# Kernel tuning notes

Measured on AMD Instinct MI355X. Metric: run time of the kernel, lower is better.

Reference implementation:

```python
import jax, jax.numpy as jnp
import numpy as np

V, D, NH, L, T, B = 32000, 768, 12, 4, 2048, 1
HD = D // NH
THETA = 10000.0
EPS = 1e-5


def setup_inputs() -> dict:
    key = jax.random.key(0)
    ks = jax.random.split(key, 12)
    s = 0.02
    return {
        "idx": jax.random.randint(ks[0], (B, T), 0, V),
        "wte": jax.random.normal(ks[1], (V, D), jnp.float32) * s,
        "ln1_w": jnp.ones((L, D), jnp.float32),
        "attn_w": jax.random.normal(ks[2], (L, 3 * D, D), jnp.float32) * s,
        "attnproj_w": jax.random.normal(ks[3], (L, D, D), jnp.float32) * s,
        "ln2_w": jnp.ones((L, D), jnp.float32),
        "fc_w": jax.random.normal(ks[4], (L, 4 * D, D), jnp.float32) * s,
        "fc_b": jnp.zeros((L, 4 * D), jnp.float32),
        "proj_w": jax.random.normal(ks[5], (L, D, 4 * D), jnp.float32) * s,
        "proj_b": jnp.zeros((L, D), jnp.float32),
        "lnf_w": jnp.ones((D,), jnp.float32),
        "unemb_b": jnp.zeros((V,), jnp.float32),
    }


def _ln(x, w):
    mu = jnp.mean(x, axis=-1, keepdims=True)
    var = jnp.mean(jnp.square(x - mu), axis=-1, keepdims=True)
    return (x - mu) * jax.lax.rsqrt(var + EPS) * w


def _rope(x, cos, sin):
    # x: [B,NH,T,HD]; cos/sin: [T,HD//2]
    x1, x2 = x[..., : HD // 2], x[..., HD // 2 :]
    return jnp.concatenate([x1 * cos - x2 * sin, x1 * sin + x2 * cos], axis=-1)


def _forward(idx, wte, ln1_w, attn_w, attnproj_w, ln2_w, fc_w, fc_b, proj_w, proj_b, lnf_w, unemb_b):
    x = wte[idx]  # [B,T,D]
    inv_freq = 1.0 / (THETA ** (jnp.arange(0, HD, 2, dtype=jnp.float32) / HD))  # [HD/2]
    t = jnp.arange(T, dtype=jnp.float32)
    freqs = jnp.outer(t, inv_freq)  # [T, HD/2]
    cos, sin = jnp.cos(freqs), jnp.sin(freqs)
    causal = jnp.tril(jnp.ones((T, T), bool))
    scale = 1.0 / jnp.sqrt(jnp.asarray(HD, x.dtype))
    for l in range(L):
        h = _ln(x, ln1_w[l])
        qkv = h @ attn_w[l].T  # [B,T,3D]
        q, k, v = jnp.split(qkv, 3, axis=-1)
        q = q.reshape(B, T, NH, HD).transpose(0, 2, 1, 3)
        k = k.reshape(B, T, NH, HD).transpose(0, 2, 1, 3)
        v = v.reshape(B, T, NH, HD).transpose(0, 2, 1, 3)
        q, k = _rope(q, cos, sin), _rope(k, cos, sin)
        att = jnp.einsum("bhqd,bhkd->bhqk", q, k) * scale
        att = jnp.where(causal, att, -jnp.inf)
        att = jax.nn.softmax(att, axis=-1)
        y = jnp.einsum("bhqk,bhkd->bhqd", att, v)
        y = y.transpose(0, 2, 1, 3).reshape(B, T, D)
        x = x + y @ attnproj_w[l].T
        h = _ln(x, ln2_w[l])
        m = jax.nn.gelu(h @ fc_w[l].T + fc_b[l], approximate=False)
        x = x + m @ proj_w[l].T + proj_b[l]
    x = _ln(x, lnf_w)
    return x @ wte.T + unemb_b  # tied unembedding, [B,T,V]


def reference(idx, wte, ln1_w, attn_w, attnproj_w, ln2_w, fc_w, fc_b, proj_w, proj_b, lnf_w, unemb_b):
    return _forward(idx, wte, ln1_w, attn_w, attnproj_w, ln2_w, fc_w, fc_b, proj_w, proj_b, lnf_w, unemb_b)
```

## Files before the change

### kernel.cpp

```cpp
#include <hip/hip_runtime.h>
#include <hip/hip_bf16.h>

typedef __bf16 bf16_t;
typedef __bf16 bf16x8 __attribute__((ext_vector_type(8)));
typedef __bf16 bf16x4 __attribute__((ext_vector_type(4)));
typedef float  f32x4  __attribute__((ext_vector_type(4)));

__device__ __forceinline__ void gl_lds16(const void* g, void* l) {
    __builtin_amdgcn_global_load_lds(
        (__attribute__((address_space(1))) void*)g,
        (__attribute__((address_space(3))) void*)l, 16, 0, 0);
}

__global__ void cvt_kernel(const float* __restrict__ in, bf16_t* __restrict__ out,
                           int n4) {
    const int i = blockIdx.x * 256 + threadIdx.x;
    if (i < n4) {
        const float4 v = ((const float4*)in)[i];
        bf16x4 o;
        o.x = (bf16_t)v.x; o.y = (bf16_t)v.y; o.z = (bf16_t)v.z; o.w = (bf16_t)v.w;
        ((bf16x4*)out)[i] = o;
    }
}

__global__ void embed_kernel(const int* __restrict__ idx,
                             const float* __restrict__ wte,
                             float* __restrict__ x) {
    const int t = blockIdx.x;
    const int row = idx[t];
    const float* w = wte + (size_t)row * 768;
    float* o = x + (size_t)t * 768;
    for (int d = threadIdx.x; d < 768; d += 256) o[d] = w[d];
}

__global__ __launch_bounds__(256) void ln_kernel(const float* __restrict__ x,
                                                 const float* __restrict__ w,
                                                 bf16_t* __restrict__ out) {
    const int t = blockIdx.x, tid = threadIdx.x;
    __shared__ float red[256];
    const float* xr = x + (size_t)t * 768;
    const float v0 = xr[tid], v1 = xr[tid + 256], v2 = xr[tid + 512];
    red[tid] = v0 + v1 + v2;
    __syncthreads();
    for (int s = 128; s > 0; s >>= 1) {
        if (tid < s) red[tid] += red[tid + s];
        __syncthreads();
    }
    const float mu = red[0] * (1.0f / 768.0f);
    __syncthreads();
    const float d0 = v0 - mu, d1 = v1 - mu, d2 = v2 - mu;
    red[tid] = d0 * d0 + d1 * d1 + d2 * d2;
    __syncthreads();
    for (int s = 128; s > 0; s >>= 1) {
        if (tid < s) red[tid] += red[tid + s];
        __syncthreads();
    }
    const float rstd = rsqrtf(red[0] * (1.0f / 768.0f) + 1e-5f);
    bf16_t* orow = out + (size_t)t * 768;
    orow[tid]       = (bf16_t)(d0 * rstd * w[tid]);
    orow[tid + 256] = (bf16_t)(d1 * rstd * w[tid + 256]);
    orow[tid + 512] = (bf16_t)(d2 * rstd * w[tid + 512]);
}

__global__ __launch_bounds__(256) void rope_prep(const float* __restrict__ qkv,
                                                 bf16_t* __restrict__ Qb,
                                                 bf16_t* __restrict__ Kb,
                                                 bf16_t* __restrict__ Vt) {
    const int t0 = blockIdx.x * 64, h = blockIdx.y;
    const int tid = threadIdx.x;
    __shared__ bf16_t vt[64][65];

    #pragma unroll
    for (int it = 0; it < 16; ++it) {
        const int item = it * 256 + tid;
        const int tl = item >> 6;
        const int which = (item >> 5) & 1;
        const int i = item & 31;
        const float* src = qkv + (size_t)(t0 + tl) * 2304 + which * 768 + h * 64;
        const float inv_freq = __powf(10000.0f, -(float)i * (1.0f / 32.0f));
        const float ang = (float)(t0 + tl) * inv_freq;
        float s, c;
        __sincosf(ang, &s, &c);
        const float x1 = src[i], x2 = src[i + 32];
        bf16_t* dst = (which ? Kb : Qb) + ((size_t)h * 2048 + t0 + tl) * 64;
        const float sc = which ? 1.0f : 0.125f;
        dst[i]      = (bf16_t)((x1 * c - x2 * s) * sc);
        dst[i + 32] = (bf16_t)((x1 * s + x2 * c) * sc);
    }

    #pragma unroll
    for (int pass = 0; pass < 4; ++pass) {
        const int r = pass * 16 + (tid >> 4);
        const int c = (tid & 15) * 4;
        const float4 v = *(const float4*)(qkv + (size_t)(t0 + r) * 2304 + 1536 + h * 64 + c);
        vt[c + 0][r] = (bf16_t)v.x;
        vt[c + 1][r] = (bf16_t)v.y;
        vt[c + 2][r] = (bf16_t)v.z;
        vt[c + 3][r] = (bf16_t)v.w;
    }
    __syncthreads();
    #pragma unroll
    for (int pass = 0; pass < 2; ++pass) {
        const int d = pass * 32 + (tid >> 3);
        const int k8 = (tid & 7) * 8;
        bf16x8 vv;
        #pragma unroll
        for (int j = 0; j < 8; ++j) vv[j] = vt[d][k8 + j];
        *(bf16x8*)(Vt + ((size_t)h * 64 + d) * 2048 + t0 + k8) = vv;
    }
}

__global__ __launch_bounds__(256) void attn_mfma(const bf16_t* __restrict__ Qb,
                                                 const bf16_t* __restrict__ Kb,
                                                 const bf16_t* __restrict__ Vt,
                                                 bf16_t* __restrict__ y) {
    const int qt = (int)gridDim.x - 1 - (int)blockIdx.x;
    const int h  = blockIdx.y;
    const int q0 = qt * 64;
    const int tid = threadIdx.x;
    const int w = tid >> 6, lane = tid & 63;
    const int lg = lane >> 4;
    const int ll = lane & 15;

    __shared__ bf16_t Ks[64 * 64];
    __shared__ bf16_t Vs[64 * 64];
    __shared__ bf16_t Ps[64 * 64];

    bf16x8 aq0, aq1;
    {
        const bf16_t* qp = Qb + ((size_t)h * 2048 + q0 + w * 16 + ll) * 64 + lg * 8;
        aq0 = *(const bf16x8*)qp;
        aq1 = *(const bf16x8*)(qp + 32);
    }

    f32x4 o[4];
    #pragma unroll
    for (int i = 0; i < 4; ++i) o[i] = (f32x4)(0.0f);
    float m_i[4], l_i[4];
    #pragma unroll
    for (int r = 0; r < 4; ++r) { m_i[r] = -3e38f; l_i[r] = 0.0f; }

    const int srow0 = tid >> 3;
    const int srow1 = srow0 + 32;
    const int sc16  = tid & 7;

    const bf16_t* Kbase = Kb + (size_t)h * 2048 * 64;
    const bf16_t* Vbase = Vt + (size_t)h * 64 * 2048;

    for (int kt = 0; kt <= qt; ++kt) {
        __syncthreads();
        {
            const bf16_t* kg = Kbase + (size_t)(kt * 64) * 64;
            const bf16x8 k0 = *(const bf16x8*)(kg + srow0 * 64 + sc16 * 8);
            const bf16x8 k1 = *(const bf16x8*)(kg + srow1 * 64 + sc16 * 8);
            const bf16_t* vg = Vbase + kt * 64;
            const bf16x8 v0 = *(const bf16x8*)(vg + (size_t)srow0 * 2048 + sc16 * 8);
            const bf16x8 v1 = *(const bf16x8*)(vg + (size_t)srow1 * 2048 + sc16 * 8);
            *(bf16x8*)((char*)(Ks + srow0 * 64) + ((sc16 * 16) ^ ((srow0 & 7) << 4))) = k0;
            *(bf16x8*)((char*)(Ks + srow1 * 64) + ((sc16 * 16) ^ ((srow1 & 7) << 4))) = k1;
            *(bf16x8*)((char*)(Vs + srow0 * 64) + ((sc16 * 16) ^ ((srow0 & 7) << 4))) = v0;
            *(bf16x8*)((char*)(Vs + srow1 * 64) + ((sc16 * 16) ^ ((srow1 & 7) << 4))) = v1;
        }
        __syncthreads();

        f32x4 sacc[4];
        #pragma unroll
        for (int kb = 0; kb < 4; ++kb) {
            const int krow = kb * 16 + ll;
            const char* kr = (const char*)(Ks + krow * 64);
            const int sw = (krow & 7) << 4;
            const bf16x8 b0 = *(const bf16x8*)(kr + ((lg * 16) ^ sw));
            const bf16x8 b1 = *(const bf16x8*)(kr + ((64 + lg * 16) ^ sw));
            sacc[kb] = __builtin_amdgcn_mfma_f32_16x16x32_bf16(aq0, b0, (f32x4)(0.0f), 0, 0, 0);
            sacc[kb] = __builtin_amdgcn_mfma_f32_16x16x32_bf16(aq1, b1, sacc[kb], 0, 0, 0);
        }

        float sc_[4][4];
        const bool diag = (kt == qt);
        #pragma unroll
        for (int kb = 0; kb < 4; ++kb) {
            #pragma unroll
            for (int r = 0; r < 4; ++r) {
                float v = sacc[kb][r];
                if (diag && (kb * 16 + ll) > (w * 16 + lg * 4 + r)) v = -3e38f;
                sc_[kb][r] = v;
            }
        }
        float rmax[4];
        #pragma unroll
        for (int r = 0; r < 4; ++r)
            rmax[r] = fmaxf(fmaxf(sc_[0][r], sc_[1][r]), fmaxf(sc_[2][r], sc_[3][r]));
        #pragma unroll
        for (int st = 0; st < 4; ++st) {
            const int off = 1 << st;
            #pragma unroll
            for (int r = 0; r < 4; ++r)
                rmax[r] = fmaxf(rmax[r], __shfl_xor(rmax[r], off));
        }
        float alpha[4], rsum[4];
        #pragma unroll
        for (int r = 0; r < 4; ++r) {
            const float mn = fmaxf(m_i[r], rmax[r]);
            alpha[r] = __expf(m_i[r] - mn);
            m_i[r] = mn;
            rsum[r] = 0.0f;
        }
        #pragma unroll
        for (int kb = 0; kb < 4; ++kb) {
            #pragma unroll
            for (int r = 0; r < 4; ++r) {
                const float p = __expf(sc_[kb][r] - m_i[r]);
                sc_[kb][r] = p;
                rsum[r] += p;
            }
        }
        #pragma unroll
        for (int st = 0; st < 4; ++st) {
            const int off = 1 << st;
            #pragma unroll
            for (int r = 0; r < 4; ++r)
                rsum[r] += __shfl_xor(rsum[r], off);
        }
        #pragma unroll
        for (int r = 0; r < 4; ++r) l_i[r] = l_i[r] * alpha[r] + rsum[r];

        #pragma unroll
        for (int r = 0; r < 4; ++r) {
            const int prow = w * 16 + lg * 4 + r;
            char* pb = (char*)(Ps + prow * 64);
            const int sw = (prow & 7) << 4;
            #pragma unroll
            for (int kb = 0; kb < 4; ++kb)
                *(bf16_t*)(pb + (((kb * 16 + ll) * 2) ^ sw)) = (bf16_t)sc_[kb][r];
        }

        #pragma unroll
        for (int db = 0; db < 4; ++db)
            #pragma unroll
            for (int r = 0; r < 4; ++r) o[db][r] *= alpha[r];

        #pragma unroll
        for (int ks = 0; ks < 2; ++ks) {
            const int arow = w * 16 + ll;
            const bf16x8 ap = *(const bf16x8*)((const char*)(Ps + arow * 64) +
                                ((ks * 64 + lg * 16) ^ ((arow & 7) << 4)));
            #pragma unroll
            for (int db = 0; db < 4; ++db) {
                const int vrow = db * 16 + ll;
                const bf16x8 bv = *(const bf16x8*)((const char*)(Vs + vrow * 64) +
                                    ((ks * 64 + lg * 16) ^ ((vrow & 7) << 4)));
                o[db] = __builtin_amdgcn_mfma_f32_16x16x32_bf16(ap, bv, o[db], 0, 0, 0);
            }
        }
    }

    #pragma unroll
    for (int r = 0; r < 4; ++r) {
        const float inv = 1.0f / l_i[r];
        bf16_t* yo = y + (size_t)(q0 + w * 16 + lg * 4 + r) * 768 + h * 64 + ll;
        #pragma unroll
        for (int db = 0; db < 4; ++db)
            yo[db * 16] = (bf16_t)(o[db][r] * inv);
    }
}

template <int FLAGS, int BM>
__global__ __launch_bounds__(256) void gemm_bt(const bf16_t* __restrict__ A,
                                               const bf16_t* __restrict__ B,
                                               const float* __restrict__ bias,
                                               float* __restrict__ C32,
                                               bf16_t* __restrict__ Cb,
                                               int M, int N, int K) {
    constexpr bool HAS_BIAS = (FLAGS & 1) != 0;
    constexpr bool HAS_RES  = (FLAGS & 2) != 0;
    constexpr bool HAS_GELU = (FLAGS & 4) != 0;
    constexpr bool OUT_BF16 = (FLAGS & 8) != 0;
    constexpr bool UNEMB    = (FLAGS & 16) != 0;
    constexpr int  WM       = (BM == 128) ? 64 : 32;
    constexpr int  MI       = WM / 16;

    __shared__ bf16_t As[BM * 32];
    __shared__ bf16_t Bs[128 * 32];

    const int tid = threadIdx.x;
    const int w = tid >> 6, lane = tid & 63;
    const int bm = (UNEMB ? blockIdx.x : blockIdx.y) * BM;
    const int bn = (UNEMB ? blockIdx.y : blockIdx.x) * 128;
    const int wm = (w >> 1) * WM, wn = (w & 1) * 64;

    const int sc = (lane & 3) * 8;
    const int srB = w * 32 + (lane >> 2);
    const bf16_t* gB0 = B + (size_t)(bn + srB) * K + sc;
    const bf16_t* gB1 = gB0 + (size_t)16 * K;
    bf16_t* lB0 = Bs + (w * 32) * 32;
    bf16_t* lB1 = lB0 + 16 * 32;
    const int srA = (BM == 128) ? srB : (w * 16 + (lane >> 2));
    const bf16_t* gA0 = A + (size_t)(bm + srA) * K + sc;
    const bf16_t* gA1 = gA0 + (size_t)16 * K;
    bf16_t* lA0 = As + ((BM == 128) ? (w * 32) * 32 : (w * 16) * 32);
    bf16_t* lA1 = lA0 + 16 * 32;

    const int mrow  = lane & 15;
    const int khalf = (lane >> 4) * 8;

    f32x4 acc[MI][4];
    #pragma unroll
    for (int i = 0; i < MI; ++i)
        #pragma unroll
        for (int j = 0; j < 4; ++j) acc[i][j] = (f32x4)(0.0f);

    for (int k0 = 0; k0 < K; k0 += 32) {
        __syncthreads();
        gl_lds16(gA0 + k0, lA0);
        if constexpr (BM == 128) gl_lds16(gA1 + k0, lA1);
        gl_lds16(gB0 + k0, lB0);
        gl_lds16(gB1 + k0, lB1);
        __syncthreads();
        bf16x8 af[MI], bfr[4];
        #pragma unroll
        for (int i = 0; i < MI; ++i)
            af[i] = *(const bf16x8*)(As + (wm + i * 16 + mrow) * 32 + khalf);
        #pragma unroll
        for (int j = 0; j < 4; ++j)
            bfr[j] = *(const bf16x8*)(Bs + (wn + j * 16 + mrow) * 32 + khalf);
        #pragma unroll
        for (int i = 0; i < MI; ++i)
            #pragma unroll
            for (int j = 0; j < 4; ++j)
                acc[i][j] = __builtin_amdgcn_mfma_f32_16x16x32_bf16(
                    af[i], bfr[j], acc[i][j], 0, 0, 0);
    }

    const int ccol = lane & 15;
    const int crow = (lane >> 4) * 4;
    #pragma unroll
    for (int i = 0; i < MI; ++i) {
        #pragma unroll
        for (int j = 0; j < 4; ++j) {
            const int col = bn + wn + j * 16 + ccol;
            #pragma unroll
            for (int r = 0; r < 4; ++r) {
                const int row = bm + wm + i * 16 + crow + r;
                float v = acc[i][j][r];
                if constexpr (HAS_BIAS) v += bias[col];
                if constexpr (HAS_GELU) v = 0.5f * v * (1.0f + erff(v * 0.70710678f));
                const size_t off = (size_t)row * N + col;
                if constexpr (HAS_RES) v += C32[off];
                if constexpr (OUT_BF16) Cb[off] = (bf16_t)v;
                else if constexpr (UNEMB) __builtin_nontemporal_store(v, &C32[off]);
                else C32[off] = v;
            }
        }
    }
}

extern "C" void kernel_launch(void* const* d_in, const int* in_sizes, int n_in,
                              void* d_out, int out_size, void* d_ws, size_t ws_size,
                              hipStream_t stream) {
    const int T = 2048, D = 768, NH = 12, L = 4, V = 32000;
    const int D3 = 3 * D, D4 = 4 * D;

    const int*   idx        = (const int*)d_in[0];
    const float* wte        = (const float*)d_in[1];
    const float* ln1_w      = (const float*)d_in[2];
    const float* attn_w     = (const float*)d_in[3];
    const float* attnproj_w = (const float*)d_in[4];
    const float* ln2_w      = (const float*)d_in[5];
    const float* fc_w       = (const float*)d_in[6];
    const float* fc_b       = (const float*)d_in[7];
    const float* proj_w     = (const float*)d_in[8];
    const float* proj_b     = (const float*)d_in[9];
    const float* lnf_w      = (const float*)d_in[10];
    const float* unemb_b    = (const float*)d_in[11];
    float* out = (float*)d_out;

    char* p = (char*)d_ws;
    float*  X      = (float*)p;   p += (size_t)T * D * 4;
    bf16_t* Hb     = (bf16_t*)p;  p += (size_t)T * D * 2;
    float*  QKV    = (float*)p;
    bf16_t* Mb     = (bf16_t*)p;  p += (size_t)T * D3 * 4;
    bf16_t* wte_b  = (bf16_t*)p;  p += (size_t)V * D * 2;
    bf16_t* w_attn = (bf16_t*)p;  p += (size_t)D3 * D * 2;
    bf16_t* w_apr  = (bf16_t*)p;  p += (size_t)D * D * 2;
    bf16_t* w_fc   = (bf16_t*)p;  p += (size_t)D4 * D * 2;
    bf16_t* w_proj = (bf16_t*)p;  p += (size_t)D * D4 * 2;

    bf16_t* Qb  = wte_b;
    bf16_t* Kbf = Qb  + (size_t)NH * T * 64;
    bf16_t* Vtg = Kbf + (size_t)NH * T * 64;

    embed_kernel<<<T, 256, 0, stream>>>(idx, wte, X);

    for (int l = 0; l < L; ++l) {
        int n4;
        n4 = D3 * D / 4;
        cvt_kernel<<<(n4 + 255) / 256, 256, 0, stream>>>(attn_w + (size_t)l * D3 * D, w_attn, n4);
        n4 = D * D / 4;
        cvt_kernel<<<(n4 + 255) / 256, 256, 0, stream>>>(attnproj_w + (size_t)l * D * D, w_apr, n4);
        n4 = D4 * D / 4;
        cvt_kernel<<<(n4 + 255) / 256, 256, 0, stream>>>(fc_w + (size_t)l * D4 * D, w_fc, n4);
        n4 = D * D4 / 4;
        cvt_kernel<<<(n4 + 255) / 256, 256, 0, stream>>>(proj_w + (size_t)l * D * D4, w_proj, n4);

        ln_kernel<<<T, 256, 0, stream>>>(X, ln1_w + (size_t)l * D, Hb);
        gemm_bt<0, 128><<<dim3(D3 / 128, T / 128), 256, 0, stream>>>(
            Hb, w_attn, nullptr, QKV, nullptr, T, D3, D);
        rope_prep<<<dim3(T / 64, NH), 256, 0, stream>>>(QKV, Qb, Kbf, Vtg);
        attn_mfma<<<dim3(T / 64, NH), 256, 0, stream>>>(Qb, Kbf, Vtg, Hb);
        gemm_bt<2, 64><<<dim3(D / 128, T / 64), 256, 0, stream>>>(
            Hb, w_apr, nullptr, X, nullptr, T, D, D);
        ln_kernel<<<T, 256, 0, stream>>>(X, ln2_w + (size_t)l * D, Hb);
        gemm_bt<13, 128><<<dim3(D4 / 128, T / 128), 256, 0, stream>>>(
            Hb, w_fc, fc_b + (size_t)l * D4, nullptr, Mb, T, D4, D);
        gemm_bt<3, 64><<<dim3(D / 128, T / 64), 256, 0, stream>>>(
            Mb, w_proj, proj_b + (size_t)l * D, X, nullptr, T, D, D4);
    }

    ln_kernel<<<T, 256, 0, stream>>>(X, lnf_w, Hb);
    {
        const int n4 = V * D / 4;
        cvt_kernel<<<(n4 + 255) / 256, 256, 0, stream>>>(wte, wte_b, n4);
    }
    gemm_bt<17, 128><<<dim3(T / 128, V / 128), 256, 0, stream>>>(
        Hb, wte_b, unemb_b, out, nullptr, T, V, D);
}
```

Measured before the change: 1.423 ms.

## Double-buffer GEMM LDS loads, stage unembed epilogue, batch weight conversion, precompute RoPE table

The GEMM main loop now double-buffers LDS tiles with global_load_lds prefetch and explicit vmcnt waits, so loads of the next K slice overlap MFMA work on the current one. The unembedding epilogue stages accumulators through LDS so each lane writes contiguous 16-byte nontemporal stores. The four per-layer weight conversions are merged into one launch, RoPE cos/sin values are precomputed once into a table, and the embedding copy is vectorised. The changes double GEMM LDS usage, which may lower occupancy, and the hand-written waitcnt counts must match the number of loads issued per stage.

```diff
diff --git a/kernel.cpp b/kernel.cpp
--- a/kernel.cpp
+++ b/kernel.cpp
@@ -10,6 +10,13 @@
     __builtin_amdgcn_global_load_lds(
         (__attribute__((address_space(1))) void*)g,
         (__attribute__((address_space(3))) void*)l, 16, 0, 0);
+}
+
+template <int N>
+__device__ __forceinline__ void wait_vm() {
+    if constexpr (N == 0)      asm volatile("s_waitcnt vmcnt(0)" ::: "memory");
+    else if constexpr (N == 3) asm volatile("s_waitcnt vmcnt(3)" ::: "memory");
+    else                       asm volatile("s_waitcnt vmcnt(4)" ::: "memory");
 }
 
 __global__ void cvt_kernel(const float* __restrict__ in, bf16_t* __restrict__ out,
@@ -23,14 +30,52 @@
     }
 }
 
+__global__ void cvt4_kernel(const float* __restrict__ s0, const float* __restrict__ s1,
+                            const float* __restrict__ s2, const float* __restrict__ s3,
+                            bf16_t* __restrict__ d0, bf16_t* __restrict__ d1,
+                            bf16_t* __restrict__ d2, bf16_t* __restrict__ d3,
+                            int n0, int n1, int n2, int n3) {
+    int j = blockIdx.x * 256 + threadIdx.x;
+    const float* s; bf16_t* d;
+    if (j < n0) { s = s0; d = d0; }
+    else {
+        j -= n0;
+        if (j < n1) { s = s1; d = d1; }
+        else {
+            j -= n1;
+            if (j < n2) { s = s2; d = d2; }
+            else {
+                j -= n2;
+                if (j >= n3) return;
+                s = s3; d = d3;
+            }
+        }
+    }
+    const float4 v = ((const float4*)s)[j];
+    bf16x4 o;
+    o.x = (bf16_t)v.x; o.y = (bf16_t)v.y; o.z = (bf16_t)v.z; o.w = (bf16_t)v.w;
+    ((bf16x4*)d)[j] = o;
+}
+
+__global__ void rope_table(float* __restrict__ tab) {
+    const int i = blockIdx.x * 256 + threadIdx.x;
+    const int t = i >> 5, f = i & 31;
+    const float inv_freq = __powf(10000.0f, -(float)f * (1.0f / 32.0f));
+    const float ang = (float)t * inv_freq;
+    float s, c;
+    __sincosf(ang, &s, &c);
+    tab[2 * i]     = c;
+    tab[2 * i + 1] = s;
+}
+
 __global__ void embed_kernel(const int* __restrict__ idx,
                              const float* __restrict__ wte,
                              float* __restrict__ x) {
     const int t = blockIdx.x;
     const int row = idx[t];
-    const float* w = wte + (size_t)row * 768;
-    float* o = x + (size_t)t * 768;
-    for (int d = threadIdx.x; d < 768; d += 256) o[d] = w[d];
+    const float4* w = (const float4*)(wte + (size_t)row * 768);
+    float4* o = (float4*)(x + (size_t)t * 768);
+    if (threadIdx.x < 192) o[threadIdx.x] = w[threadIdx.x];
 }
 
 __global__ __launch_bounds__(256) void ln_kernel(const float* __restrict__ x,
@@ -63,6 +108,7 @@
 }
 
 __global__ __launch_bounds__(256) void rope_prep(const float* __restrict__ qkv,
+                                                 const float* __restrict__ tab,
                                                  bf16_t* __restrict__ Qb,
                                                  bf16_t* __restrict__ Kb,
                                                  bf16_t* __restrict__ Vt) {
@@ -77,10 +123,8 @@
         const int which = (item >> 5) & 1;
         const int i = item & 31;
         const float* src = qkv + (size_t)(t0 + tl) * 2304 + which * 768 + h * 64;
-        const float inv_freq = __powf(10000.0f, -(float)i * (1.0f / 32.0f));
-        const float ang = (float)(t0 + tl) * inv_freq;
-        float s, c;
-        __sincosf(ang, &s, &c);
+        const float2 cs = ((const float2*)tab)[(t0 + tl) * 32 + i];
+        const float c = cs.x, s = cs.y;
         const float x1 = src[i], x2 = src[i + 32];
         bf16_t* dst = (which ? Kb : Qb) + ((size_t)h * 2048 + t0 + tl) * 64;
         const float sc = which ? 1.0f : 0.125f;
@@ -278,9 +322,13 @@
     constexpr bool UNEMB    = (FLAGS & 16) != 0;
     constexpr int  WM       = (BM == 128) ? 64 : 32;
     constexpr int  MI       = WM / 16;
-
-    __shared__ bf16_t As[BM * 32];
-    __shared__ bf16_t Bs[128 * 32];
+    constexpr int  NLOADS   = (BM == 128) ? 4 : 3;
+
+    __shared__ bf16_t smem[2 * (BM + 128) * 32];
+    bf16_t* As0 = smem;
+    bf16_t* Bs0 = As0 + BM * 32;
+    bf16_t* As1 = Bs0 + 128 * 32;
+    bf16_t* Bs1 = As1 + BM * 32;
 
     const int tid = threadIdx.x;
     const int w = tid >> 6, lane = tid & 63;
@@ -292,13 +340,11 @@
     const int srB = w * 32 + (lane >> 2);
     const bf16_t* gB0 = B + (size_t)(bn + srB) * K + sc;
     const bf16_t* gB1 = gB0 + (size_t)16 * K;
-    bf16_t* lB0 = Bs + (w * 32) * 32;
-    bf16_t* lB1 = lB0 + 16 * 32;
     const int srA = (BM == 128) ? srB : (w * 16 + (lane >> 2));
     const bf16_t* gA0 = A + (size_t)(bm + srA) * K + sc;
     const bf16_t* gA1 = gA0 + (size_t)16 * K;
-    bf16_t* lA0 = As + ((BM == 128) ? (w * 32) * 32 : (w * 16) * 32);
-    bf16_t* lA1 = lA0 + 16 * 32;
+    const int ldsA = ((BM == 128) ? (w * 32) : (w * 16)) * 32;
+    const int ldsB = (w * 32) * 32;
 
     const int mrow  = lane & 15;
     const int khalf = (lane >> 4) * 8;
@@ -309,30 +355,79 @@
         #pragma unroll
         for (int j = 0; j < 4; ++j) acc[i][j] = (f32x4)(0.0f);
 
-    for (int k0 = 0; k0 < K; k0 += 32) {
-        __syncthreads();
-        gl_lds16(gA0 + k0, lA0);
-        if constexpr (BM == 128) gl_lds16(gA1 + k0, lA1);
-        gl_lds16(gB0 + k0, lB0);
-        gl_lds16(gB1 + k0, lB1);
-        __syncthreads();
+    auto stage = [&](bf16_t* Ap, bf16_t* Bp, int kk) {
+        gl_lds16(gA0 + kk, Ap + ldsA);
+        if constexpr (BM == 128) gl_lds16(gA1 + kk, Ap + ldsA + 16 * 32);
+        gl_lds16(gB0 + kk, Bp + ldsB);
+        gl_lds16(gB1 + kk, Bp + ldsB + 16 * 32);
+    };
+    auto compute = [&](const bf16_t* Ap, const bf16_t* Bp) {
         bf16x8 af[MI], bfr[4];
         #pragma unroll
         for (int i = 0; i < MI; ++i)
-            af[i] = *(const bf16x8*)(As + (wm + i * 16 + mrow) * 32 + khalf);
+            af[i] = *(const bf16x8*)(Ap + (wm + i * 16 + mrow) * 32 + khalf);
         #pragma unroll
         for (int j = 0; j < 4; ++j)
-            bfr[j] = *(const bf16x8*)(Bs + (wn + j * 16 + mrow) * 32 + khalf);
+            bfr[j] = *(const bf16x8*)(Bp + (wn + j * 16 + mrow) * 32 + khalf);
         #pragma unroll
         for (int i = 0; i < MI; ++i)
             #pragma unroll
             for (int j = 0; j < 4; ++j)
                 acc[i][j] = __builtin_amdgcn_mfma_f32_16x16x32_bf16(
                     af[i], bfr[j], acc[i][j], 0, 0, 0);
+    };
+
+    stage(As0, Bs0, 0);
+    for (int k0 = 0; k0 < K; k0 += 64) {
+        stage(As1, Bs1, k0 + 32);
+        wait_vm<NLOADS>();
+        __builtin_amdgcn_s_barrier();
+        __builtin_amdgcn_sched_barrier(0);
+        compute(As0, Bs0);
+        __builtin_amdgcn_sched_barrier(0);
+        __builtin_amdgcn_s_barrier();
+        const bool more = (k0 + 64) < K;
+        if (more) stage(As0, Bs0, k0 + 64);
+        if (more) wait_vm<NLOADS>(); else wait_vm<0>();
+        __builtin_amdgcn_s_barrier();
+        __builtin_amdgcn_sched_barrier(0);
+        compute(As1, Bs1);
+        __builtin_amdgcn_sched_barrier(0);
+        __builtin_amdgcn_s_barrier();
     }
 
     const int ccol = lane & 15;
     const int crow = (lane >> 4) * 4;
+
+    if constexpr (UNEMB) {
+        __syncthreads();
+        float* ep = (float*)smem + (size_t)w * (16 * 68);
+        const int rl = lane >> 2, c4 = (lane & 3) * 16;
+        #pragma unroll
+        for (int i = 0; i < MI; ++i) {
+            #pragma unroll
+            for (int j = 0; j < 4; ++j) {
+                #pragma unroll
+                for (int r = 0; r < 4; ++r) {
+                    float v = acc[i][j][r];
+                    if constexpr (HAS_BIAS) v += bias[bn + wn + j * 16 + ccol];
+                    ep[(crow + r) * 68 + j * 16 + ccol] = v;
+                }
+            }
+            asm volatile("s_waitcnt lgkmcnt(0)" ::: "memory");
+            __builtin_amdgcn_sched_barrier(0);
+            float* dst = C32 + (size_t)(bm + wm + i * 16 + rl) * N + bn + wn + c4;
+            #pragma unroll
+            for (int c = 0; c < 4; ++c) {
+                const f32x4 v4 = *(const f32x4*)(ep + rl * 68 + c4 + c * 4);
+                __builtin_nontemporal_store(v4, (f32x4*)(dst + c * 4));
+            }
+            asm volatile("s_waitcnt lgkmcnt(0)" ::: "memory");
+            __builtin_amdgcn_sched_barrier(0);
+        }
+        return;
+    }
+
     #pragma unroll
     for (int i = 0; i < MI; ++i) {
         #pragma unroll
@@ -347,7 +442,6 @@
                 const size_t off = (size_t)row * N + col;
                 if constexpr (HAS_RES) v += C32[off];
                 if constexpr (OUT_BF16) Cb[off] = (bf16_t)v;
-                else if constexpr (UNEMB) __builtin_nontemporal_store(v, &C32[off]);
                 else C32[off] = v;
             }
         }
@@ -384,28 +478,28 @@
     bf16_t* w_apr  = (bf16_t*)p;  p += (size_t)D * D * 2;
     bf16_t* w_fc   = (bf16_t*)p;  p += (size_t)D4 * D * 2;
     bf16_t* w_proj = (bf16_t*)p;  p += (size_t)D * D4 * 2;
+    float*  rtab   = (float*)p;   p += (size_t)T * 32 * 2 * 4;
 
     bf16_t* Qb  = wte_b;
     bf16_t* Kbf = Qb  + (size_t)NH * T * 64;
     bf16_t* Vtg = Kbf + (size_t)NH * T * 64;
 
     embed_kernel<<<T, 256, 0, stream>>>(idx, wte, X);
+    rope_table<<<T * 32 / 256, 256, 0, stream>>>(rtab);
+
+    const int na = D3 * D / 4, nb = D * D / 4, nc = D4 * D / 4, nd = D * D4 / 4;
+    const int ntot = na + nb + nc + nd;
 
     for (int l = 0; l < L; ++l) {
-        int n4;
-        n4 = D3 * D / 4;
-        cvt_kernel<<<(n4 + 255) / 256, 256, 0, stream>>>(attn_w + (size_t)l * D3 * D, w_attn, n4);
-        n4 = D * D / 4;
-        cvt_kernel<<<(n4 + 255) / 256, 256, 0, stream>>>(attnproj_w + (size_t)l * D * D, w_apr, n4);
-        n4 = D4 * D / 4;
-        cvt_kernel<<<(n4 + 255) / 256, 256, 0, stream>>>(fc_w + (size_t)l * D4 * D, w_fc, n4);
-        n4 = D * D4 / 4;
-        cvt_kernel<<<(n4 + 255) / 256, 256, 0, stream>>>(proj_w + (size_t)l * D * D4, w_proj, n4);
+        cvt4_kernel<<<(ntot + 255) / 256, 256, 0, stream>>>(
+            attn_w + (size_t)l * D3 * D, attnproj_w + (size_t)l * D * D,
+            fc_w + (size_t)l * D4 * D, proj_w + (size_t)l * D * D4,
+            w_attn, w_apr, w_fc, w_proj, na, nb, nc, nd);
 
         ln_kernel<<<T, 256, 0, stream>>>(X, ln1_w + (size_t)l * D, Hb);
         gemm_bt<0, 128><<<dim3(D3 / 128, T / 128), 256, 0, stream>>>(
             Hb, w_attn, nullptr, QKV, nullptr, T, D3, D);
-        rope_prep<<<dim3(T / 64, NH), 256, 0, stream>>>(QKV, Qb, Kbf, Vtg);
+        rope_prep<<<dim3(T / 64, NH), 256, 0, stream>>>(QKV, rtab, Qb, Kbf, Vtg);
         attn_mfma<<<dim3(T / 64, NH), 256, 0, stream>>>(Qb, Kbf, Vtg, Hb);
         gemm_bt<2, 64><<<dim3(D / 128, T / 64), 256, 0, stream>>>(
             Hb, w_apr, nullptr, X, nullptr, T, D, D);
```

Result: slower. 1.583 ms (+11.2%).
